# Kernel optimization log

Measured on AMD Instinct MI355X. Metric: run time of the kernel, lower is better.

## Reference

```python
import jax, jax.numpy as jnp
import numpy as np

TWO_PI = 2.0 * np.pi
SMOOTH = 0.12  # smoothing_factor default

N_STATIONS = 100000
N_TIME = 1000
K = 8


def _spatial_smooth(param, idx, w, is_phase=False, s=SMOOTH):
    # param: [N] (or [N,C]); idx: [N,K] int; w: [N,K] row-normalized
    nb = param[idx]  # [N,K] or [N,K,C]
    if param.ndim == 2:
        w = w[..., None]
    if is_phase:
        # circular mean via unit-complex average, expressed with real atan2
        re = (1.0 - s) * jnp.cos(param) + s * jnp.sum(w * jnp.cos(nb), axis=1)
        im = (1.0 - s) * jnp.sin(param) + s * jnp.sum(w * jnp.sin(nb), axis=1)
        return jnp.arctan2(im, re)
    return (1.0 - s) * param + s * jnp.sum(w * nb, axis=1)


def setup_inputs() -> dict:
    key = jax.random.key(0)
    ks = jax.random.split(key, 10)
    time_vector = jnp.arange(N_TIME, dtype=jnp.float32) / 365.25  # years
    constant_offset = jnp.zeros((N_STATIONS,), jnp.float32)
    linear_trend = jax.random.normal(ks[0], (N_STATIONS,), jnp.float32) * 5.0
    seasonal_amplitudes = jnp.ones((N_STATIONS, 3), jnp.float32) * 8.0
    seasonal_phases = jax.random.uniform(ks[1], (N_STATIONS, 3), jnp.float32) * TWO_PI
    residual_amplitudes = jnp.ones((N_STATIONS, 2), jnp.float32) * 1.5
    residual_phases = jax.random.uniform(ks[2], (N_STATIONS, 2), jnp.float32) * TWO_PI
    residual_periods = jnp.array([180.0, 730.0], jnp.float32)
    periods = jnp.array([0.25, 0.5, 1.0], jnp.float32)
    neighbor_indices = jax.random.randint(ks[3], (N_STATIONS, K), 0, N_STATIONS)
    raw_w = jax.random.uniform(ks[4], (N_STATIONS, K), jnp.float32)
    neighbor_weights = raw_w / (jnp.sum(raw_w, axis=1, keepdims=True) + 1e-6)
    return {
        "time_vector": time_vector,
        "constant_offset": constant_offset,
        "linear_trend": linear_trend,
        "seasonal_amplitudes": seasonal_amplitudes,
        "seasonal_phases": seasonal_phases,
        "residual_amplitudes": residual_amplitudes,
        "residual_phases": residual_phases,
        "residual_periods": residual_periods,
        "periods": periods,
        "neighbor_indices": neighbor_indices,
        "neighbor_weights": neighbor_weights,
    }


def reference(time_vector, constant_offset, linear_trend, seasonal_amplitudes,
              seasonal_phases, residual_amplitudes, residual_phases,
              residual_periods, periods, neighbor_indices, neighbor_weights):
    t = time_vector[None, :]  # [1,T] broadcast over stations
    signals = constant_offset[:, None] + linear_trend[:, None] * t  # [N,T]
    # batched spatial smoothing across all 3 seasonal channels at once
    sm_amp = _spatial_smooth(seasonal_amplitudes, neighbor_indices, neighbor_weights)            # [N,3]
    sm_phase = _spatial_smooth(seasonal_phases, neighbor_indices, neighbor_weights, is_phase=True)  # [N,3]
    for i in range(3):  # fixed small set of periods
        freq = 1.0 / periods[i]
        signals = signals + sm_amp[:, i:i+1] * jnp.sin(TWO_PI * freq * t + sm_phase[:, i:i+1])
    for i in range(2):
        freq = 1.0 / residual_periods[i]
        signals = signals + residual_amplitudes[:, i:i+1] * jnp.sin(TWO_PI * freq * t + residual_phases[:, i:i+1])
    return signals
```

## Files before the change

### kernel.cpp

```cpp
#include <hip/hip_runtime.h>

typedef float f32x4 __attribute__((ext_vector_type(4)));
typedef float f32x2 __attribute__((ext_vector_type(2)));

#define NSEAS 3
#define NRES  2
#define NCOMP 5
#define KNB   8
#define TWO_PI_F 6.28318530717958647692f
#define SPB  100
#define BSIG 512

static __device__ __forceinline__ f32x2 bc2(float x) {
    f32x2 r; r.x = x; r.y = x; return r;
}

__global__ __launch_bounds__(BSIG, 4) void fused_insar_kernel(
    const float* __restrict__ time_vector,
    const float* __restrict__ constant_offset,
    const float* __restrict__ linear_trend,
    const float* __restrict__ seas_amp,
    const float* __restrict__ seas_phase,
    const float* __restrict__ res_amp,
    const float* __restrict__ res_phase,
    const float* __restrict__ res_periods,
    const float* __restrict__ periods,
    const int*   __restrict__ nb_idx,
    const float* __restrict__ nb_w,
    float* __restrict__ out,
    int N, int T)
{
    __shared__ __align__(16) float sp[SPB * 12];

    const int tid   = threadIdx.x;
    const int stBeg = blockIdx.x * SPB;
    const int nst   = min(SPB, N - stBeg);

    if (tid < nst) {
        const int st = stBeg + tid;
        const float S = 0.12f, OMS = 1.0f - 0.12f;

        const int4*  ip = reinterpret_cast<const int4*>(nb_idx + st * KNB);
        const f32x4* wp = reinterpret_cast<const f32x4*>(nb_w + st * KNB);
        int4  i0 = ip[0], i1 = ip[1];
        f32x4 w0 = wp[0], w1 = wp[1];
        int   idx[KNB] = {i0.x, i0.y, i0.z, i0.w, i1.x, i1.y, i1.z, i1.w};
        float w[KNB]   = {w0.x, w0.y, w0.z, w0.w, w1.x, w1.y, w1.z, w1.w};

        float accA[NSEAS]  = {0.f, 0.f, 0.f};
        float accRe[NSEAS] = {0.f, 0.f, 0.f};
        float accIm[NSEAS] = {0.f, 0.f, 0.f};

        #pragma unroll
        for (int k = 0; k < KNB; ++k) {
            int nb = idx[k];
            #pragma unroll
            for (int i = 0; i < NSEAS; ++i) {
                float a = seas_amp[nb * NSEAS + i];
                float p = seas_phase[nb * NSEAS + i];
                float spn, cpn;
                __sincosf(p, &spn, &cpn);
                accA[i]  = fmaf(w[k], a,   accA[i]);
                accRe[i] = fmaf(w[k], cpn, accRe[i]);
                accIm[i] = fmaf(w[k], spn, accIm[i]);
            }
        }

        float outp[12];
        outp[0] = constant_offset[st];
        outp[1] = linear_trend[st];

        #pragma unroll
        for (int i = 0; i < NSEAS; ++i) {
            float smA = OMS * seas_amp[st * NSEAS + i] + S * accA[i];
            float spn, cpn;
            __sincosf(seas_phase[st * NSEAS + i], &spn, &cpn);
            float re = OMS * cpn + S * accRe[i];
            float im = OMS * spn + S * accIm[i];
            float r   = sqrtf(re * re + im * im);
            float inv = smA / fmaxf(r, 1e-30f);
            outp[2 + 2 * i] = re * inv;
            outp[3 + 2 * i] = im * inv;
        }

        #pragma unroll
        for (int i = 0; i < NRES; ++i) {
            float a = res_amp[st * NRES + i];
            float spn, cpn;
            __sincosf(res_phase[st * NRES + i], &spn, &cpn);
            outp[2 + 2 * (NSEAS + i)] = a * cpn;
            outp[3 + 2 * (NSEAS + i)] = a * spn;
        }

        f32x4* po = reinterpret_cast<f32x4*>(sp + tid * 12);
        po[0] = f32x4{outp[0], outp[1], outp[2],  outp[3]};
        po[1] = f32x4{outp[4], outp[5], outp[6],  outp[7]};
        po[2] = f32x4{outp[8], outp[9], outp[10], outp[11]};
    }

    const int tid8 = tid & 255;
    const int half = tid >> 8;
    const int t0   = tid8 * 4;
    const bool active = (t0 + 3) < T;

    f32x2 tv2[2];
    f32x2 sT2[NCOMP][2], cT2[NCOMP][2];
    if (active) {
        f32x4 t4 = *reinterpret_cast<const f32x4*>(time_vector + t0);
        tv2[0].x = t4.x; tv2[0].y = t4.y;
        tv2[1].x = t4.z; tv2[1].y = t4.w;
        #pragma unroll
        for (int c = 0; c < NCOMP; ++c) {
            float f = (c < NSEAS) ? (1.0f / periods[c])
                                  : (1.0f / res_periods[c - NSEAS]);
            float wc = TWO_PI_F * f;
            float s0, c0, s1, c1, s2, c2, s3, c3;
            __sincosf(wc * t4.x, &s0, &c0);
            __sincosf(wc * t4.y, &s1, &c1);
            __sincosf(wc * t4.z, &s2, &c2);
            __sincosf(wc * t4.w, &s3, &c3);
            sT2[c][0].x = s0; sT2[c][0].y = s1;
            sT2[c][1].x = s2; sT2[c][1].y = s3;
            cT2[c][0].x = c0; cT2[c][0].y = c1;
            cT2[c][1].x = c2; cT2[c][1].y = c3;
        }
    }

    __syncthreads();

    auto dost = [&](int s, f32x4 P0, f32x4 P1, f32x4 P2) {
        f32x2 of = bc2(P0.x), tr = bc2(P0.y);
        f32x2 a0 = __builtin_elementwise_fma(tr, tv2[0], of);
        f32x2 a1 = __builtin_elementwise_fma(tr, tv2[1], of);
        a0 = __builtin_elementwise_fma(bc2(P0.z), sT2[0][0], a0);
        a1 = __builtin_elementwise_fma(bc2(P0.z), sT2[0][1], a1);
        a0 = __builtin_elementwise_fma(bc2(P0.w), cT2[0][0], a0);
        a1 = __builtin_elementwise_fma(bc2(P0.w), cT2[0][1], a1);
        a0 = __builtin_elementwise_fma(bc2(P1.x), sT2[1][0], a0);
        a1 = __builtin_elementwise_fma(bc2(P1.x), sT2[1][1], a1);
        a0 = __builtin_elementwise_fma(bc2(P1.y), cT2[1][0], a0);
        a1 = __builtin_elementwise_fma(bc2(P1.y), cT2[1][1], a1);
        a0 = __builtin_elementwise_fma(bc2(P1.z), sT2[2][0], a0);
        a1 = __builtin_elementwise_fma(bc2(P1.z), sT2[2][1], a1);
        a0 = __builtin_elementwise_fma(bc2(P1.w), cT2[2][0], a0);
        a1 = __builtin_elementwise_fma(bc2(P1.w), cT2[2][1], a1);
        a0 = __builtin_elementwise_fma(bc2(P2.x), sT2[3][0], a0);
        a1 = __builtin_elementwise_fma(bc2(P2.x), sT2[3][1], a1);
        a0 = __builtin_elementwise_fma(bc2(P2.y), cT2[3][0], a0);
        a1 = __builtin_elementwise_fma(bc2(P2.y), cT2[3][1], a1);
        a0 = __builtin_elementwise_fma(bc2(P2.z), sT2[4][0], a0);
        a1 = __builtin_elementwise_fma(bc2(P2.z), sT2[4][1], a1);
        a0 = __builtin_elementwise_fma(bc2(P2.w), cT2[4][0], a0);
        a1 = __builtin_elementwise_fma(bc2(P2.w), cT2[4][1], a1);
        f32x4 o; o.x = a0.x; o.y = a0.y; o.z = a1.x; o.w = a1.y;
        *reinterpret_cast<f32x4*>(out + (size_t)(stBeg + s) * T + t0) = o;
    };

    const f32x4* spv = reinterpret_cast<const f32x4*>(sp);

    if (active) {
        int s = half;
        for (; s + 2 < nst; s += 4) {
            f32x4 A0 = spv[3 * s],       A1 = spv[3 * s + 1],       A2 = spv[3 * s + 2];
            f32x4 B0 = spv[3 * (s + 2)], B1 = spv[3 * (s + 2) + 1], B2 = spv[3 * (s + 2) + 2];
            dost(s, A0, A1, A2);
            dost(s + 2, B0, B1, B2);
        }
        for (; s < nst; s += 2) {
            dost(s, spv[3 * s], spv[3 * s + 1], spv[3 * s + 2]);
        }
    } else if (t0 < T) {
        for (int s = half; s < nst; s += 2) {
            const f32x4* pv = spv + 3 * s;
            f32x4 P0 = pv[0], P1 = pv[1], P2 = pv[2];
            float off = P0.x, trend = P0.y;
            float cs[NCOMP] = {P0.z, P1.x, P1.z, P2.x, P2.z};
            float cc[NCOMP] = {P0.w, P1.y, P1.w, P2.y, P2.w};
            for (int j = 0; j < 4 && t0 + j < T; ++j) {
                int t = t0 + j;
                float tt = time_vector[t];
                float acc = fmaf(trend, tt, off);
                for (int i = 0; i < NCOMP; ++i) {
                    float f = (i < NSEAS) ? (1.0f / periods[i])
                                          : (1.0f / res_periods[i - NSEAS]);
                    float sv, cv;
                    __sincosf(TWO_PI_F * f * tt, &sv, &cv);
                    acc = fmaf(cs[i], sv, acc);
                    acc = fmaf(cc[i], cv, acc);
                }
                out[(size_t)(stBeg + s) * T + t] = acc;
            }
        }
    }
}

extern "C" void kernel_launch(void* const* d_in, const int* in_sizes, int n_in,
                              void* d_out, int out_size, void* d_ws, size_t ws_size,
                              hipStream_t stream) {
    const float* time_vector     = (const float*)d_in[0];
    const float* constant_offset = (const float*)d_in[1];
    const float* linear_trend    = (const float*)d_in[2];
    const float* seas_amp        = (const float*)d_in[3];
    const float* seas_phase      = (const float*)d_in[4];
    const float* res_amp         = (const float*)d_in[5];
    const float* res_phase       = (const float*)d_in[6];
    const float* res_periods     = (const float*)d_in[7];
    const float* periods         = (const float*)d_in[8];
    const int*   nb_idx          = (const int*)d_in[9];
    const float* nb_w            = (const float*)d_in[10];

    int T = in_sizes[0];
    int N = in_sizes[1];

    float* out = (float*)d_out;

    int grid = (N + SPB - 1) / SPB;
    fused_insar_kernel<<<grid, BSIG, 0, stream>>>(
        time_vector, constant_offset, linear_trend,
        seas_amp, seas_phase, res_amp, res_phase,
        res_periods, periods, nb_idx, nb_w,
        out, N, T);
}
```

Baseline: 98.46 us.

## Remap output phase so each lane covers 16 time samples, each wave a station slice

The block shrinks from 512 to 256 threads. In the output phase each of the four waves now owns a contiguous quarter of the block's stations, and each lane covers 16 consecutive time samples instead of 4. The per-sample sin/cos basis is computed once per lane into registers and reused across all of that wave's stations, which adds more independent FMAs per station row. In exchange the register footprint is large (about 180 VGPRs for the basis), which lowers occupancy, and each store instruction now writes with a 64-byte stride across lanes rather than fully contiguous float4 lanes. That store pattern could hurt what is essentially a write-bandwidth-bound kernel.

Measured after the change: 213.9 us. 117% more time.

```diff
diff --git a/kernel.cpp b/kernel.cpp
--- a/kernel.cpp
+++ b/kernel.cpp
@@ -9,13 +9,13 @@
 #define KNB   8
 #define TWO_PI_F 6.28318530717958647692f
 #define SPB  100
-#define BSIG 512
+#define BSIG 256
 
 static __device__ __forceinline__ f32x2 bc2(float x) {
     f32x2 r; r.x = x; r.y = x; return r;
 }
 
-__global__ __launch_bounds__(BSIG, 4) void fused_insar_kernel(
+__global__ __launch_bounds__(BSIG) void fused_insar_kernel(
     const float* __restrict__ time_vector,
     const float* __restrict__ constant_offset,
     const float* __restrict__ linear_trend,
@@ -98,97 +98,106 @@
         po[2] = f32x4{outp[8], outp[9], outp[10], outp[11]};
     }
 
-    const int tid8 = tid & 255;
-    const int half = tid >> 8;
-    const int t0   = tid8 * 4;
-    const bool active = (t0 + 3) < T;
-
-    f32x2 tv2[2];
-    f32x2 sT2[NCOMP][2], cT2[NCOMP][2];
-    if (active) {
-        f32x4 t4 = *reinterpret_cast<const f32x4*>(time_vector + t0);
-        tv2[0].x = t4.x; tv2[0].y = t4.y;
-        tv2[1].x = t4.z; tv2[1].y = t4.w;
-        #pragma unroll
-        for (int c = 0; c < NCOMP; ++c) {
-            float f = (c < NSEAS) ? (1.0f / periods[c])
-                                  : (1.0f / res_periods[c - NSEAS]);
-            float wc = TWO_PI_F * f;
-            float s0, c0, s1, c1, s2, c2, s3, c3;
-            __sincosf(wc * t4.x, &s0, &c0);
-            __sincosf(wc * t4.y, &s1, &c1);
-            __sincosf(wc * t4.z, &s2, &c2);
-            __sincosf(wc * t4.w, &s3, &c3);
-            sT2[c][0].x = s0; sT2[c][0].y = s1;
-            sT2[c][1].x = s2; sT2[c][1].y = s3;
-            cT2[c][0].x = c0; cT2[c][0].y = c1;
-            cT2[c][1].x = c2; cT2[c][1].y = c3;
+    const int lane = tid & 63;
+    const int wv   = tid >> 6;
+    const int e0   = lane * 16;
+    int nel = T - e0;
+    nel = nel < 0 ? 0 : (nel > 16 ? 16 : nel);
+    const int nq  = nel >> 2;
+
+    float fr[NCOMP];
+    fr[0] = 1.0f / periods[0];
+    fr[1] = 1.0f / periods[1];
+    fr[2] = 1.0f / periods[2];
+    fr[3] = 1.0f / res_periods[0];
+    fr[4] = 1.0f / res_periods[1];
+
+    f32x2 tvp[8];
+    f32x2 sb[NCOMP][8], cb[NCOMP][8];
+    #pragma unroll
+    for (int q = 0; q < 4; ++q) {
+        if (q < nq) {
+            f32x4 t4 = *reinterpret_cast<const f32x4*>(time_vector + e0 + 4 * q);
+            tvp[2 * q].x     = t4.x; tvp[2 * q].y     = t4.y;
+            tvp[2 * q + 1].x = t4.z; tvp[2 * q + 1].y = t4.w;
+            #pragma unroll
+            for (int c = 0; c < NCOMP; ++c) {
+                float wc = TWO_PI_F * fr[c];
+                float s0, c0, s1, c1, s2, c2, s3, c3;
+                __sincosf(wc * t4.x, &s0, &c0);
+                __sincosf(wc * t4.y, &s1, &c1);
+                __sincosf(wc * t4.z, &s2, &c2);
+                __sincosf(wc * t4.w, &s3, &c3);
+                sb[c][2 * q].x = s0;     sb[c][2 * q].y = s1;
+                sb[c][2 * q + 1].x = s2; sb[c][2 * q + 1].y = s3;
+                cb[c][2 * q].x = c0;     cb[c][2 * q].y = c1;
+                cb[c][2 * q + 1].x = c2; cb[c][2 * q + 1].y = c3;
+            }
         }
     }
 
     __syncthreads();
 
-    auto dost = [&](int s, f32x4 P0, f32x4 P1, f32x4 P2) {
-        f32x2 of = bc2(P0.x), tr = bc2(P0.y);
-        f32x2 a0 = __builtin_elementwise_fma(tr, tv2[0], of);
-        f32x2 a1 = __builtin_elementwise_fma(tr, tv2[1], of);
-        a0 = __builtin_elementwise_fma(bc2(P0.z), sT2[0][0], a0);
-        a1 = __builtin_elementwise_fma(bc2(P0.z), sT2[0][1], a1);
-        a0 = __builtin_elementwise_fma(bc2(P0.w), cT2[0][0], a0);
-        a1 = __builtin_elementwise_fma(bc2(P0.w), cT2[0][1], a1);
-        a0 = __builtin_elementwise_fma(bc2(P1.x), sT2[1][0], a0);
-        a1 = __builtin_elementwise_fma(bc2(P1.x), sT2[1][1], a1);
-        a0 = __builtin_elementwise_fma(bc2(P1.y), cT2[1][0], a0);
-        a1 = __builtin_elementwise_fma(bc2(P1.y), cT2[1][1], a1);
-        a0 = __builtin_elementwise_fma(bc2(P1.z), sT2[2][0], a0);
-        a1 = __builtin_elementwise_fma(bc2(P1.z), sT2[2][1], a1);
-        a0 = __builtin_elementwise_fma(bc2(P1.w), cT2[2][0], a0);
-        a1 = __builtin_elementwise_fma(bc2(P1.w), cT2[2][1], a1);
-        a0 = __builtin_elementwise_fma(bc2(P2.x), sT2[3][0], a0);
-        a1 = __builtin_elementwise_fma(bc2(P2.x), sT2[3][1], a1);
-        a0 = __builtin_elementwise_fma(bc2(P2.y), cT2[3][0], a0);
-        a1 = __builtin_elementwise_fma(bc2(P2.y), cT2[3][1], a1);
-        a0 = __builtin_elementwise_fma(bc2(P2.z), sT2[4][0], a0);
-        a1 = __builtin_elementwise_fma(bc2(P2.z), sT2[4][1], a1);
-        a0 = __builtin_elementwise_fma(bc2(P2.w), cT2[4][0], a0);
-        a1 = __builtin_elementwise_fma(bc2(P2.w), cT2[4][1], a1);
-        f32x4 o; o.x = a0.x; o.y = a0.y; o.z = a1.x; o.w = a1.y;
-        *reinterpret_cast<f32x4*>(out + (size_t)(stBeg + s) * T + t0) = o;
-    };
-
     const f32x4* spv = reinterpret_cast<const f32x4*>(sp);
-
-    if (active) {
-        int s = half;
-        for (; s + 2 < nst; s += 4) {
-            f32x4 A0 = spv[3 * s],       A1 = spv[3 * s + 1],       A2 = spv[3 * s + 2];
-            f32x4 B0 = spv[3 * (s + 2)], B1 = spv[3 * (s + 2) + 1], B2 = spv[3 * (s + 2) + 2];
-            dost(s, A0, A1, A2);
-            dost(s + 2, B0, B1, B2);
-        }
-        for (; s < nst; s += 2) {
-            dost(s, spv[3 * s], spv[3 * s + 1], spv[3 * s + 2]);
-        }
-    } else if (t0 < T) {
-        for (int s = half; s < nst; s += 2) {
-            const f32x4* pv = spv + 3 * s;
-            f32x4 P0 = pv[0], P1 = pv[1], P2 = pv[2];
-            float off = P0.x, trend = P0.y;
-            float cs[NCOMP] = {P0.z, P1.x, P1.z, P2.x, P2.z};
-            float cc[NCOMP] = {P0.w, P1.y, P1.w, P2.y, P2.w};
-            for (int j = 0; j < 4 && t0 + j < T; ++j) {
-                int t = t0 + j;
-                float tt = time_vector[t];
-                float acc = fmaf(trend, tt, off);
-                for (int i = 0; i < NCOMP; ++i) {
-                    float f = (i < NSEAS) ? (1.0f / periods[i])
-                                          : (1.0f / res_periods[i - NSEAS]);
+    const int per = (nst + 3) >> 2;
+    const int sBegW = wv * per;
+    const int sEndW = min(sBegW + per, nst);
+
+    for (int s = sBegW; s < sEndW; ++s) {
+        f32x4 P0 = spv[3 * s], P1 = spv[3 * s + 1], P2 = spv[3 * s + 2];
+        float cs[NCOMP] = {P0.z, P1.x, P1.z, P2.x, P2.z};
+        float cc[NCOMP] = {P0.w, P1.y, P1.w, P2.y, P2.w};
+        float* orow = out + (size_t)(stBeg + s) * T + e0;
+
+        if (nel == 16) {
+            f32x2 a[8];
+            f32x2 of = bc2(P0.x), tr = bc2(P0.y);
+            #pragma unroll
+            for (int p = 0; p < 8; ++p)
+                a[p] = __builtin_elementwise_fma(tr, tvp[p], of);
+            #pragma unroll
+            for (int c = 0; c < NCOMP; ++c) {
+                f32x2 vs = bc2(cs[c]), vc = bc2(cc[c]);
+                #pragma unroll
+                for (int p = 0; p < 8; ++p) {
+                    a[p] = __builtin_elementwise_fma(vs, sb[c][p],
+                           __builtin_elementwise_fma(vc, cb[c][p], a[p]));
+                }
+            }
+            #pragma unroll
+            for (int q = 0; q < 4; ++q) {
+                f32x4 o;
+                o.x = a[2 * q].x; o.y = a[2 * q].y;
+                o.z = a[2 * q + 1].x; o.w = a[2 * q + 1].y;
+                *reinterpret_cast<f32x4*>(orow + 4 * q) = o;
+            }
+        } else if (nel > 0) {
+            for (int q = 0; q < nq; ++q) {
+                f32x2 of = bc2(P0.x), tr = bc2(P0.y);
+                f32x2 a0 = __builtin_elementwise_fma(tr, tvp[2 * q], of);
+                f32x2 a1 = __builtin_elementwise_fma(tr, tvp[2 * q + 1], of);
+                #pragma unroll
+                for (int c = 0; c < NCOMP; ++c) {
+                    f32x2 vs = bc2(cs[c]), vc = bc2(cc[c]);
+                    a0 = __builtin_elementwise_fma(vs, sb[c][2 * q],
+                         __builtin_elementwise_fma(vc, cb[c][2 * q], a0));
+                    a1 = __builtin_elementwise_fma(vs, sb[c][2 * q + 1],
+                         __builtin_elementwise_fma(vc, cb[c][2 * q + 1], a1));
+                }
+                f32x4 o; o.x = a0.x; o.y = a0.y; o.z = a1.x; o.w = a1.y;
+                *reinterpret_cast<f32x4*>(orow + 4 * q) = o;
+            }
+            for (int j = nq * 4; j < nel; ++j) {
+                float tt = time_vector[e0 + j];
+                float acc = fmaf(P0.y, tt, P0.x);
+                #pragma unroll
+                for (int c = 0; c < NCOMP; ++c) {
                     float sv, cv;
-                    __sincosf(TWO_PI_F * f * tt, &sv, &cv);
-                    acc = fmaf(cs[i], sv, acc);
-                    acc = fmaf(cc[i], cv, acc);
+                    __sincosf(TWO_PI_F * fr[c] * tt, &sv, &cv);
+                    acc = fmaf(cs[c], sv, acc);
+                    acc = fmaf(cc[c], cv, acc);
                 }
-                out[(size_t)(stBeg + s) * T + t] = acc;
+                orow[j] = acc;
             }
         }
     }
```
